# Optimization experiments

Hardware: AMD Instinct MI355X
Metric: run time of the kernel (lower is better)

The kernel has to match this reference:

```python
import jax, jax.numpy as jnp
import numpy as np
from jax import lax

BN_EPS = 1e-3  # keras BatchNormalization default

def _conv(x, w):
    # x: (N,H,W,Cin), w: (kh,kw,Cin,Cout), 'same' padding, stride 1
    return lax.conv_general_dilated(x, w, (1, 1), 'SAME',
                                    dimension_numbers=('NHWC', 'HWIO', 'NHWC'))

def _hard_sigmoid(x):  # keras ConvLSTM2D default recurrent_activation
    return jnp.clip(0.2 * x + 0.5, 0.0, 1.0)

def _convlstm(x, Wx, Wh, b, return_sequences):
    # x: (B,T,H,W,Cin); Wx: (3,3,Cin,4F); Wh: (3,3,F,4F); gates order i,f,c,o
    B, T, H, W, Cin = x.shape
    F = Wh.shape[2]
    # precompute input-to-gate convs for all timesteps at once (one big conv)
    gx = _conv(x.reshape(B * T, H, W, Cin), Wx) + b
    gx = gx.reshape(B, T, H, W, 4 * F).transpose(1, 0, 2, 3, 4)  # (T,B,H,W,4F)
    h0 = jnp.zeros((B, H, W, F), x.dtype)
    c0 = jnp.zeros((B, H, W, F), x.dtype)

    def step(carry, gxt):
        h, c = carry
        z = gxt + _conv(h, Wh)
        zi, zf, zc, zo = jnp.split(z, 4, axis=-1)
        c = _hard_sigmoid(zf) * c + _hard_sigmoid(zi) * jnp.tanh(zc)
        h = _hard_sigmoid(zo) * jnp.tanh(c)
        return (h, c), h

    (hT, _), hs = lax.scan(step, (h0, c0), gx)
    if return_sequences:
        return hs.transpose(1, 0, 2, 3, 4)  # (B,T,H,W,F)
    return hT  # (B,H,W,F)

def _bn(x, gamma, beta, mean, var):
    return (x - mean) * (gamma * lax.rsqrt(var + BN_EPS)) + beta

def _pool_thw(x):  # MaxPool3D(pool_size=(1,2,2))
    B, T, H, W, C = x.shape
    return x.reshape(B, T, H // 2, 2, W // 2, 2, C).max(axis=(3, 5))

def _pool_hw(x):  # MaxPool2D()
    B, H, W, C = x.shape
    return x.reshape(B, H // 2, 2, W // 2, 2, C).max(axis=(2, 4))

def setup_inputs() -> dict:
    key = jax.random.key(0)
    ks = jax.random.split(key, 16)
    s = 0.05  # weight scale
    d = {
        'x':   jax.random.normal(ks[0], (8, 12, 64, 64, 3), jnp.float32),
        'W1x': jax.random.normal(ks[1], (3, 3, 3, 64), jnp.float32) * s,
        'W1h': jax.random.normal(ks[2], (3, 3, 16, 64), jnp.float32) * s,
        'b1':  jnp.zeros((64,), jnp.float32),
        'g1':  jnp.ones((16,), jnp.float32),
        'be1': jnp.zeros((16,), jnp.float32),
        'm1':  jax.random.normal(ks[3], (16,), jnp.float32) * 0.1,
        'v1':  jax.random.uniform(ks[4], (16,), jnp.float32) + 0.5,
        'W2x': jax.random.normal(ks[5], (3, 3, 16, 128), jnp.float32) * s,
        'W2h': jax.random.normal(ks[6], (3, 3, 32, 128), jnp.float32) * s,
        'b2':  jnp.zeros((128,), jnp.float32),
        'g2':  jnp.ones((32,), jnp.float32),
        'be2': jnp.zeros((32,), jnp.float32),
        'm2':  jax.random.normal(ks[7], (32,), jnp.float32) * 0.1,
        'v2':  jax.random.uniform(ks[8], (32,), jnp.float32) + 0.5,
        'W3x': jax.random.normal(ks[9], (3, 3, 32, 256), jnp.float32) * s,
        'W3h': jax.random.normal(ks[10], (3, 3, 64, 256), jnp.float32) * s,
        'b3':  jnp.zeros((256,), jnp.float32),
        'Wd1': jax.random.normal(ks[11], (4096, 10000), jnp.float32) * 0.01,
        'bd1': jnp.zeros((10000,), jnp.float32),
        'Wd2': jax.random.normal(ks[12], (10000, 1000), jnp.float32) * 0.01,
        'bd2': jnp.zeros((1000,), jnp.float32),
        'Wd3': jax.random.normal(ks[13], (1000, 100), jnp.float32) * 0.03,
        'bd3': jnp.zeros((100,), jnp.float32),
        'Wd4': jax.random.normal(ks[14], (100, 10), jnp.float32) * 0.1,
        'bd4': jnp.zeros((10,), jnp.float32),
        'Wc':  jax.random.normal(ks[15], (10, 1), jnp.float32) * 0.3,
        'bc':  jnp.zeros((1,), jnp.float32),
    }
    return d

def reference(x, W1x, W1h, b1, g1, be1, m1, v1,
              W2x, W2h, b2, g2, be2, m2, v2,
              W3x, W3h, b3,
              Wd1, bd1, Wd2, bd2, Wd3, bd3, Wd4, bd4, Wc, bc):
    h = _convlstm(x, W1x, W1h, b1, True)          # (B,12,64,64,16)
    h = _bn(h, g1, be1, m1, v1)
    h = _pool_thw(h)                              # (B,12,32,32,16)
    h = _convlstm(h, W2x, W2h, b2, True)          # (B,12,32,32,32)
    h = _bn(h, g2, be2, m2, v2)
    h = _pool_thw(h)                              # (B,12,16,16,32)
    h = _convlstm(h, W3x, W3h, b3, False)         # (B,16,16,64)
    h = _pool_hw(h)                               # (B,8,8,64)
    h = h.reshape(h.shape[0], -1)                 # (B,4096)
    h = h @ Wd1 + bd1
    h = h @ Wd2 + bd2
    h = h @ Wd3 + bd3
    h = h @ Wd4 + bd4
    return h @ Wc + bc                            # (B,1)
```

## Files before the change

### kernel.cpp

```cpp
#include <hip/hip_runtime.h>
#include <hip/hip_bf16.h>
#include <math.h>

__global__ void transpose_wx(const float* __restrict__ src, float* __restrict__ dst,
                             int Cin, int CinP, int Cout)
{
  int i = blockIdx.x * 256 + threadIdx.x;
  int total = 9 * Cout * CinP;
  if (i >= total) return;
  int j = i & 3; int rem = i >> 2;
  int co = rem % Cout; rem /= Cout;
  int c4c = rem % (CinP / 4); int tap = rem / (CinP / 4);
  int c = c4c * 4 + j;
  dst[i] = (c < Cin) ? src[((size_t)tap * Cin + c) * Cout + co] : 0.f;
}

__global__ void transpose_wh(const float* __restrict__ src, float* __restrict__ dst, int F)
{
  int i = blockIdx.x * 256 + threadIdx.x;
  int total = 9 * 4 * F * F;
  if (i >= total) return;
  int j = i & 3; int rem = i >> 2;
  int f = rem % F; rem /= F;
  int c4c = rem % (F / 4); rem /= (F / 4);
  int g = rem & 3; int tap = rem >> 2;
  int c = c4c * 4 + j;
  dst[i] = src[((size_t)tap * F + c) * 4 * F + g * F + f];
}

template<int H, int W, int Cin, int Cout, int TH, int TW, int COL, int NG>
__global__ __launch_bounds__(256) void conv3x3_bias(
    const float* __restrict__ in, const float* __restrict__ wtT,
    const float* __restrict__ bias, float* __restrict__ out)
{
  static_assert(COL * NG == Cout, "cout coverage");
  constexpr int CIN_P = (Cin % 4 == 0) ? Cin : ((Cin + 3) / 4) * 4;
  constexpr int TILES_X = W / TW, TILES_Y = H / TH;
  constexpr int PAD_W = TW + 2, PAD_H = TH + 2;
  constexpr int LDS_N = PAD_H * PAD_W * CIN_P;
  constexpr int NPG = 256 / COL;
  constexpr int PPT = TH * TW / NPG;
  __shared__ __align__(16) float tile[LDS_N];

  int blk = blockIdx.x;
  int n = blk / (TILES_X * TILES_Y);
  int trem = blk % (TILES_X * TILES_Y);
  int ty = trem / TILES_X, tx = trem % TILES_X;
  int y0 = ty * TH, x0 = tx * TW;
  const float* inN = in + (size_t)n * H * W * Cin;

  for (int i = threadIdx.x; i < LDS_N; i += 256) {
    int ci = i % CIN_P; int rem = i / CIN_P;
    int xx = rem % PAD_W; int yy = rem / PAD_W;
    int gy = y0 + yy - 1, gx = x0 + xx - 1;
    float v = 0.f;
    if (ci < Cin && gy >= 0 && gy < H && gx >= 0 && gx < W)
      v = inN[((size_t)gy * W + gx) * Cin + ci];
    tile[i] = v;
  }
  __syncthreads();

  int cobase = threadIdx.x % COL;
  int pg = threadIdx.x / COL;
  float* outN = out + (size_t)n * H * W * Cout;

  float acc[NG][PPT];
#pragma unroll
  for (int g = 0; g < NG; ++g) {
    float bco = bias[g * COL + cobase];
#pragma unroll
    for (int j = 0; j < PPT; ++j) acc[g][j] = bco;
  }

  const float4* wt4 = (const float4*)wtT;
#pragma unroll
  for (int kh = 0; kh < 3; ++kh)
#pragma unroll
  for (int kw = 0; kw < 3; ++kw) {
    const float4* wtap = wt4 + (size_t)(kh * 3 + kw) * (CIN_P / 4) * Cout;
#pragma unroll 1
    for (int c4 = 0; c4 < CIN_P; c4 += 4) {
      const float4* wrow = wtap + (size_t)(c4 / 4) * Cout + cobase;
      float4 w[NG];
#pragma unroll
      for (int g = 0; g < NG; ++g) w[g] = wrow[g * COL];
#pragma unroll
      for (int j = 0; j < PPT; ++j) {
        int p = pg * PPT + j;
        int ly = p / TW, lx = p % TW;
        const float4 h4 = *(const float4*)&tile[((ly + kh) * PAD_W + (lx + kw)) * CIN_P + c4];
#pragma unroll
        for (int g = 0; g < NG; ++g)
          acc[g][j] += h4.x * w[g].x + h4.y * w[g].y + h4.z * w[g].z + h4.w * w[g].w;
      }
    }
  }

#pragma unroll
  for (int j = 0; j < PPT; ++j) {
    int p = pg * PPT + j;
    int ly = p / TW, lx = p % TW;
    float* op = &outN[((size_t)(y0 + ly) * W + (x0 + lx)) * Cout + cobase];
#pragma unroll
    for (int g = 0; g < NG; ++g) op[g * COL] = acc[g][j];
  }
}

__device__ __forceinline__ float hsig(float x) {
  return fminf(fmaxf(0.2f * x + 0.5f, 0.f), 1.f);
}

template<int H, int W, int F, int TH, int TW>
__global__ __launch_bounds__(256) void lstm_step(
    const float* __restrict__ gx, long gx_bstride,
    const float* __restrict__ hprev, long hp_bstride,
    const float* __restrict__ whT,
    float* __restrict__ c,
    float* __restrict__ hout, long ho_bstride,
    int first)
{
  constexpr int TILES_X = W / TW, TILES_Y = H / TH;
  constexpr int PAD_W = TW + 2, PAD_H = TH + 2;
  constexpr int LDS_N = PAD_H * PAD_W * F;
  __shared__ __align__(16) float tile[LDS_N];

  int blk = blockIdx.x;
  int b = blk / (TILES_X * TILES_Y);
  int trem = blk % (TILES_X * TILES_Y);
  int ty = trem / TILES_X, tx = trem % TILES_X;
  int y0 = ty * TH, x0 = tx * TW;

  if (first) {
    for (int i = threadIdx.x; i < LDS_N; i += 256) tile[i] = 0.f;
  } else {
    const float* hb = hprev + (size_t)b * hp_bstride;
    for (int i = threadIdx.x; i < LDS_N; i += 256) {
      int ci = i % F; int rem = i / F;
      int xx = rem % PAD_W, yy = rem / PAD_W;
      int gy = y0 + yy - 1, gxp = x0 + xx - 1;
      float v = 0.f;
      if (gy >= 0 && gy < H && gxp >= 0 && gxp < W)
        v = hb[((size_t)gy * W + gxp) * F + ci];
      tile[i] = v;
    }
  }
  __syncthreads();

  constexpr int G = 256 / F;
  constexpr int P = TH * TW;
  constexpr int NP = P / G;
  int f = threadIdx.x % F;
  int pg = threadIdx.x / F;

  float acc[4][NP];
  const float* gxb = gx + (size_t)b * gx_bstride;
#pragma unroll
  for (int j = 0; j < NP; ++j) {
    int p = pg * NP + j;
    int gy = y0 + p / TW, gxp = x0 + p % TW;
    size_t base = ((size_t)gy * W + gxp) * 4 * F;
#pragma unroll
    for (int g = 0; g < 4; ++g) acc[g][j] = gxb[base + g * F + f];
  }

  const float4* wh4 = (const float4*)whT;
#pragma unroll
  for (int kh = 0; kh < 3; ++kh)
#pragma unroll
  for (int kw = 0; kw < 3; ++kw) {
    int tap = kh * 3 + kw;
#pragma unroll 1
    for (int c4 = 0; c4 < F; c4 += 4) {
      float4 h4[NP];
#pragma unroll
      for (int j = 0; j < NP; ++j) {
        int p = pg * NP + j;
        int ly = p / TW, lx = p % TW;
        h4[j] = *(const float4*)&tile[((ly + kh) * PAD_W + (lx + kw)) * F + c4];
      }
      float4 w0 = wh4[((size_t)(tap * 4 + 0) * (F / 4) + c4 / 4) * F + f];
      float4 w1 = wh4[((size_t)(tap * 4 + 1) * (F / 4) + c4 / 4) * F + f];
      float4 w2 = wh4[((size_t)(tap * 4 + 2) * (F / 4) + c4 / 4) * F + f];
      float4 w3 = wh4[((size_t)(tap * 4 + 3) * (F / 4) + c4 / 4) * F + f];
#pragma unroll
      for (int j = 0; j < NP; ++j) {
        acc[0][j] += h4[j].x * w0.x + h4[j].y * w0.y + h4[j].z * w0.z + h4[j].w * w0.w;
        acc[1][j] += h4[j].x * w1.x + h4[j].y * w1.y + h4[j].z * w1.z + h4[j].w * w1.w;
        acc[2][j] += h4[j].x * w2.x + h4[j].y * w2.y + h4[j].z * w2.z + h4[j].w * w2.w;
        acc[3][j] += h4[j].x * w3.x + h4[j].y * w3.y + h4[j].z * w3.z + h4[j].w * w3.w;
      }
    }
  }

  float* cb = c + (size_t)b * H * W * F;
  float* hb2 = hout + (size_t)b * ho_bstride;
#pragma unroll
  for (int j = 0; j < NP; ++j) {
    int p = pg * NP + j;
    int gy = y0 + p / TW, gxp = x0 + p % TW;
    size_t idx = ((size_t)gy * W + gxp) * F + f;
    float zi = acc[0][j], zf = acc[1][j], zc = acc[2][j], zo = acc[3][j];
    float cold = first ? 0.f : cb[idx];
    float cn = hsig(zf) * cold + hsig(zi) * tanhf(zc);
    cb[idx] = cn;
    hb2[idx] = hsig(zo) * tanhf(cn);
  }
}

__global__ void bnpool_kernel(const float* __restrict__ in,
                              const float* __restrict__ g, const float* __restrict__ be,
                              const float* __restrict__ m, const float* __restrict__ v,
                              float* __restrict__ out, int total, int H, int W, int F)
{
  int i = blockIdx.x * 256 + threadIdx.x;
  if (i >= total) return;
  int f = i % F; int rem = i / F;
  int x = rem % (W / 2); rem /= (W / 2);
  int y = rem % (H / 2); int nt = rem / (H / 2);
  float scale = g[f] * rsqrtf(v[f] + 1e-3f);
  float shift = be[f] - m[f] * scale;
  const float* base = in + (((size_t)nt * H + 2 * y) * W + 2 * x) * F + f;
  float a0 = base[0] * scale + shift;
  float a1 = base[F] * scale + shift;
  float a2 = base[(size_t)W * F] * scale + shift;
  float a3 = base[(size_t)W * F + F] * scale + shift;
  out[i] = fmaxf(fmaxf(a0, a1), fmaxf(a2, a3));
}

__global__ void poolhw_kernel(const float* __restrict__ in, float* __restrict__ out, int total)
{
  int i = blockIdx.x * 256 + threadIdx.x;
  if (i >= total) return;
  int f = i % 64; int rem = i / 64;
  int x = rem % 8; rem /= 8;
  int y = rem % 8; int b = rem / 8;
  const float* base = in + (((size_t)b * 16 + 2 * y) * 16 + 2 * x) * 64 + f;
  float a0 = base[0], a1 = base[64], a2 = base[16 * 64], a3 = base[16 * 64 + 64];
  out[i] = fmaxf(fmaxf(a0, a1), fmaxf(a2, a3));
}

__global__ __launch_bounds__(256) void dense_partial(
    const float* __restrict__ x, const float* __restrict__ w,
    float* __restrict__ part, int K, int N, int kchunk)
{
  extern __shared__ __align__(16) float xs[];
  int kb = blockIdx.y;
  int k0 = kb * kchunk;
  int klen = min(kchunk, K - k0);
  for (int i = threadIdx.x; i < klen * 8; i += 256) {
    int kk = i >> 3, b = i & 7;
    xs[i] = x[(size_t)b * K + k0 + kk];
  }
  __syncthreads();
  int co = blockIdx.x * 256 + threadIdx.x;
  if (co >= N) return;
  float acc[8];
#pragma unroll
  for (int b = 0; b < 8; ++b) acc[b] = 0.f;
  const float4* xs4 = (const float4*)xs;
  const float* wp = w + (size_t)k0 * N + co;
#pragma unroll 4
  for (int kk = 0; kk < klen; ++kk) {
    float wv = wp[(size_t)kk * N];
    float4 lo = xs4[kk * 2], hi = xs4[kk * 2 + 1];
    acc[0] += lo.x * wv; acc[1] += lo.y * wv;
    acc[2] += lo.z * wv; acc[3] += lo.w * wv;
    acc[4] += hi.x * wv; acc[5] += hi.y * wv;
    acc[6] += hi.z * wv; acc[7] += hi.w * wv;
  }
#pragma unroll
  for (int b = 0; b < 8; ++b)
    part[((size_t)kb * 8 + b) * N + co] = acc[b];
}

__global__ __launch_bounds__(256) void dense_reduce(
    const float* __restrict__ part, const float* __restrict__ bias,
    float* __restrict__ out, int N, int S)
{
  int co = blockIdx.x * 256 + threadIdx.x;
  int b = blockIdx.y;
  if (co >= N) return;
  float acc = bias[co];
#pragma unroll 4
  for (int kb = 0; kb < S; ++kb)
    acc += part[((size_t)kb * 8 + b) * N + co];
  out[(size_t)b * N + co] = acc;
}

__global__ void dense_small(const float* __restrict__ x, const float* __restrict__ w,
                            const float* __restrict__ bias, float* __restrict__ out,
                            int K, int N, int total)
{
  int idx = blockIdx.x * 256 + threadIdx.x;
  if (idx >= total) return;
  int b = idx / N, co = idx % N;
  float acc = bias[co];
  const float* xb = x + (size_t)b * K;
#pragma unroll 4
  for (int k = 0; k < K; ++k) acc += xb[k] * w[(size_t)k * N + co];
  out[idx] = acc;
}

__global__ void dense_tail(const float* __restrict__ d3,
                           const float* __restrict__ w4, const float* __restrict__ b4,
                           const float* __restrict__ wc, const float* __restrict__ bc,
                           float* __restrict__ out)
{
  __shared__ float d4[8][10];
  int t = threadIdx.x;
  if (t < 80) {
    int b = t / 10, co = t % 10;
    float acc = b4[co];
    for (int k = 0; k < 100; ++k) acc += d3[b * 100 + k] * w4[k * 10 + co];
    d4[b][co] = acc;
  }
  __syncthreads();
  if (t < 8) {
    float acc = bc[0];
    for (int j = 0; j < 10; ++j) acc += d4[t][j] * wc[j];
    out[t] = acc;
  }
}

extern "C" void kernel_launch(void* const* d_in, const int* in_sizes, int n_in,
                              void* d_out, int out_size, void* d_ws, size_t ws_size,
                              hipStream_t stream)
{
  const float* x   = (const float*)d_in[0];
  const float* W1x = (const float*)d_in[1];
  const float* W1h = (const float*)d_in[2];
  const float* b1  = (const float*)d_in[3];
  const float* g1  = (const float*)d_in[4];
  const float* be1 = (const float*)d_in[5];
  const float* m1  = (const float*)d_in[6];
  const float* v1  = (const float*)d_in[7];
  const float* W2x = (const float*)d_in[8];
  const float* W2h = (const float*)d_in[9];
  const float* b2  = (const float*)d_in[10];
  const float* g2  = (const float*)d_in[11];
  const float* be2 = (const float*)d_in[12];
  const float* m2  = (const float*)d_in[13];
  const float* v2  = (const float*)d_in[14];
  const float* W3x = (const float*)d_in[15];
  const float* W3h = (const float*)d_in[16];
  const float* b3  = (const float*)d_in[17];
  const float* Wd1 = (const float*)d_in[18];
  const float* bd1 = (const float*)d_in[19];
  const float* Wd2 = (const float*)d_in[20];
  const float* bd2 = (const float*)d_in[21];
  const float* Wd3 = (const float*)d_in[22];
  const float* bd3 = (const float*)d_in[23];
  const float* Wd4 = (const float*)d_in[24];
  const float* bd4 = (const float*)d_in[25];
  const float* Wc  = (const float*)d_in[26];
  const float* bc  = (const float*)d_in[27];

  char* ws = (char*)d_ws;
  size_t off = 0;
  auto alloc = [&](size_t bytes) { size_t r = off; off = (off + bytes + 255) & ~(size_t)255; return r; };
  size_t oR0    = alloc(100663296);
  size_t oR1    = alloc(25165824);
  size_t oR2    = alloc(6291456);
  size_t oR3    = alloc(2097152);
  size_t oh3a   = alloc(524288);
  size_t oh3b   = alloc(524288);
  size_t oflat  = alloc(131072);
  size_t od1    = alloc(320000);
  size_t od2    = alloc(32000);
  size_t od3    = alloc(3200);
  size_t oWx1T  = alloc(9216);
  size_t oWx2T  = alloc(73728);
  size_t oWx3T  = alloc(294912);
  size_t oWh1T  = alloc(36864);
  size_t oWh2T  = alloc(147456);
  size_t oWh3T  = alloc(589824);
  (void)ws_size; (void)in_sizes; (void)n_in; (void)out_size;

  float* gx1   = (float*)(ws + oR0);
  float* gx2   = (float*)(ws + oR0);
  float* gx3   = (float*)(ws + oR0);
  float* part1 = (float*)(ws + oR0);
  float* part2 = (float*)(ws + oR0 + 33554432);
  float* hseq1 = (float*)(ws + oR1);
  float* hseq2 = (float*)(ws + oR1);
  float* pool1 = (float*)(ws + oR2);
  float* pool2 = (float*)(ws + oR2);
  float* cbuf  = (float*)(ws + oR3);
  float* h3a   = (float*)(ws + oh3a);
  float* h3b   = (float*)(ws + oh3b);
  float* flat  = (float*)(ws + oflat);
  float* d1    = (float*)(ws + od1);
  float* d2    = (float*)(ws + od2);
  float* d3b   = (float*)(ws + od3);
  float* Wx1T  = (float*)(ws + oWx1T);
  float* Wx2T  = (float*)(ws + oWx2T);
  float* Wx3T  = (float*)(ws + oWx3T);
  float* Wh1T  = (float*)(ws + oWh1T);
  float* Wh2T  = (float*)(ws + oWh2T);
  float* Wh3T  = (float*)(ws + oWh3T);

  const int B = 8, T = 12;

  transpose_wx<<<(9 * 64 * 4 + 255) / 256, 256, 0, stream>>>(W1x, Wx1T, 3, 4, 64);
  transpose_wx<<<(9 * 128 * 16 + 255) / 256, 256, 0, stream>>>(W2x, Wx2T, 16, 16, 128);
  transpose_wx<<<(9 * 256 * 32 + 255) / 256, 256, 0, stream>>>(W3x, Wx3T, 32, 32, 256);
  transpose_wh<<<(9 * 4 * 16 * 16 + 255) / 256, 256, 0, stream>>>(W1h, Wh1T, 16);
  transpose_wh<<<(9 * 4 * 32 * 32 + 255) / 256, 256, 0, stream>>>(W2h, Wh2T, 32);
  transpose_wh<<<(9 * 4 * 64 * 64 + 255) / 256, 256, 0, stream>>>(W3h, Wh3T, 64);

  conv3x3_bias<64, 64, 3, 64, 4, 8, 32, 2><<<96 * 128, 256, 0, stream>>>(x, Wx1T, b1, gx1);
  {
    const long gxs = (long)T * 64 * 64 * 64;
    const long hs  = (long)T * 64 * 64 * 16;
    for (int t = 0; t < T; ++t) {
      lstm_step<64, 64, 16, 8, 8><<<B * 64, 256, 0, stream>>>(
          gx1 + (size_t)t * 64 * 64 * 64, gxs,
          t ? hseq1 + (size_t)(t - 1) * 64 * 64 * 16 : nullptr, hs,
          Wh1T, cbuf, hseq1 + (size_t)t * 64 * 64 * 16, hs, t == 0);
    }
  }
  {
    int total = B * T * 32 * 32 * 16;
    bnpool_kernel<<<(total + 255) / 256, 256, 0, stream>>>(hseq1, g1, be1, m1, v1, pool1, total, 64, 64, 16);
  }

  conv3x3_bias<32, 32, 16, 128, 4, 8, 32, 4><<<96 * 32, 256, 0, stream>>>(pool1, Wx2T, b2, gx2);
  {
    const long gxs = (long)T * 32 * 32 * 128;
    const long hs  = (long)T * 32 * 32 * 32;
    for (int t = 0; t < T; ++t) {
      lstm_step<32, 32, 32, 4, 4><<<B * 64, 256, 0, stream>>>(
          gx2 + (size_t)t * 32 * 32 * 128, gxs,
          t ? hseq2 + (size_t)(t - 1) * 32 * 32 * 32 : nullptr, hs,
          Wh2T, cbuf, hseq2 + (size_t)t * 32 * 32 * 32, hs, t == 0);
    }
  }
  {
    int total = B * T * 16 * 16 * 32;
    bnpool_kernel<<<(total + 255) / 256, 256, 0, stream>>>(hseq2, g2, be2, m2, v2, pool2, total, 32, 32, 32);
  }

  conv3x3_bias<16, 16, 32, 256, 4, 8, 64, 4><<<96 * 8, 256, 0, stream>>>(pool2, Wx3T, b3, gx3);
  {
    const long gxs = (long)T * 16 * 16 * 256;
    const long hs  = (long)16 * 16 * 64;
    for (int t = 0; t < T; ++t) {
      float* hout = (t % 2 == 0) ? h3a : h3b;
      const float* hp = (t % 2 == 0) ? h3b : h3a;
      lstm_step<16, 16, 64, 2, 4><<<B * 32, 256, 0, stream>>>(
          gx3 + (size_t)t * 16 * 16 * 256, gxs,
          t ? hp : nullptr, hs,
          Wh3T, cbuf, hout, hs, t == 0);
    }
  }
  poolhw_kernel<<<(32768 + 255) / 256, 256, 0, stream>>>(h3b, flat, 32768);

  dense_partial<<<dim3(40, 64), 256, 64 * 8 * 4, stream>>>(flat, Wd1, part1, 4096, 10000, 64);
  dense_reduce<<<dim3(40, 8), 256, 0, stream>>>(part1, bd1, d1, 10000, 64);
  dense_partial<<<dim3(4, 125), 256, 80 * 8 * 4, stream>>>(d1, Wd2, part2, 10000, 1000, 80);
  dense_reduce<<<dim3(4, 8), 256, 0, stream>>>(part2, bd2, d2, 1000, 125);
  dense_small<<<(800 + 255) / 256, 256, 0, stream>>>(d2, Wd3, bd3, d3b, 1000, 100, 800);
  dense_tail<<<1, 128, 0, stream>>>(d3b, Wd4, bd4, Wc, bc, (float*)d_out);
}
```

Before: 1.518 ms.

## Fuse ConvLSTM timesteps into persistent kernels with grid-wide atomic barriers

Replaces the per-timestep lstm_step launches with one persistent lstm_layer kernel per layer that loops over all 12 timesteps and synchronises blocks through an atomic counter barrier in global memory. The goal is to remove 36 kernel launches and their launch gaps. The six weight-transpose kernels become a single launch, and the third dense layer becomes a split-K partial/reduce pair. The grid barrier only works if every block is resident at once; the grids are 512 and 256 blocks with launch_bounds(256,2), so a co-residency failure would deadlock.

```diff
diff --git a/kernel.cpp b/kernel.cpp
--- a/kernel.cpp
+++ b/kernel.cpp
@@ -2,12 +2,10 @@
 #include <hip/hip_bf16.h>
 #include <math.h>
 
-__global__ void transpose_wx(const float* __restrict__ src, float* __restrict__ dst,
-                             int Cin, int CinP, int Cout)
-{
-  int i = blockIdx.x * 256 + threadIdx.x;
-  int total = 9 * Cout * CinP;
-  if (i >= total) return;
+__device__ __forceinline__ void wx_elem(const float* __restrict__ src,
+                                        float* __restrict__ dst, int i,
+                                        int Cin, int CinP, int Cout)
+{
   int j = i & 3; int rem = i >> 2;
   int co = rem % Cout; rem /= Cout;
   int c4c = rem % (CinP / 4); int tap = rem / (CinP / 4);
@@ -15,17 +13,31 @@
   dst[i] = (c < Cin) ? src[((size_t)tap * Cin + c) * Cout + co] : 0.f;
 }
 
-__global__ void transpose_wh(const float* __restrict__ src, float* __restrict__ dst, int F)
-{
-  int i = blockIdx.x * 256 + threadIdx.x;
-  int total = 9 * 4 * F * F;
-  if (i >= total) return;
+__device__ __forceinline__ void wh_elem(const float* __restrict__ src,
+                                        float* __restrict__ dst, int i, int F)
+{
   int j = i & 3; int rem = i >> 2;
   int f = rem % F; rem /= F;
   int c4c = rem % (F / 4); rem /= (F / 4);
   int g = rem & 3; int tap = rem >> 2;
   int c = c4c * 4 + j;
   dst[i] = src[((size_t)tap * F + c) * 4 * F + g * F + f];
+}
+
+__global__ void transpose_all(
+    const float* __restrict__ W1x, const float* __restrict__ W2x,
+    const float* __restrict__ W3x, const float* __restrict__ W1h,
+    const float* __restrict__ W2h, const float* __restrict__ W3h,
+    float* __restrict__ Wx1T, float* __restrict__ Wx2T, float* __restrict__ Wx3T,
+    float* __restrict__ Wh1T, float* __restrict__ Wh2T, float* __restrict__ Wh3T)
+{
+  int i = blockIdx.x * 256 + threadIdx.x;
+  if (i < 2304)        wx_elem(W1x, Wx1T, i,          3,  4,  64);
+  else if (i < 20736)  wx_elem(W2x, Wx2T, i - 2304,   16, 16, 128);
+  else if (i < 94464)  wx_elem(W3x, Wx3T, i - 20736,  32, 32, 256);
+  else if (i < 103680) wh_elem(W1h, Wh1T, i - 94464,  16);
+  else if (i < 140544) wh_elem(W2h, Wh2T, i - 103680, 32);
+  else if (i < 288000) wh_elem(W3h, Wh3T, i - 140544, 64);
 }
 
 template<int H, int W, int Cin, int Cout, int TH, int TW, int COL, int NG>
@@ -110,14 +122,13 @@
   return fminf(fmaxf(0.2f * x + 0.5f, 0.f), 1.f);
 }
 
-template<int H, int W, int F, int TH, int TW>
-__global__ __launch_bounds__(256) void lstm_step(
+template<int H, int W, int F, int TH, int TW, int TSEQ>
+__global__ __launch_bounds__(256, 2) void lstm_layer(
     const float* __restrict__ gx, long gx_bstride,
-    const float* __restrict__ hprev, long hp_bstride,
     const float* __restrict__ whT,
     float* __restrict__ c,
-    float* __restrict__ hout, long ho_bstride,
-    int first)
+    float* __restrict__ hseq, long h_bstride,
+    unsigned int* __restrict__ bar)
 {
   constexpr int TILES_X = W / TW, TILES_Y = H / TH;
   constexpr int PAD_W = TW + 2, PAD_H = TH + 2;
@@ -130,80 +141,97 @@
   int ty = trem / TILES_X, tx = trem % TILES_X;
   int y0 = ty * TH, x0 = tx * TW;
 
-  if (first) {
-    for (int i = threadIdx.x; i < LDS_N; i += 256) tile[i] = 0.f;
-  } else {
-    const float* hb = hprev + (size_t)b * hp_bstride;
-    for (int i = threadIdx.x; i < LDS_N; i += 256) {
-      int ci = i % F; int rem = i / F;
-      int xx = rem % PAD_W, yy = rem / PAD_W;
-      int gy = y0 + yy - 1, gxp = x0 + xx - 1;
-      float v = 0.f;
-      if (gy >= 0 && gy < H && gxp >= 0 && gxp < W)
-        v = hb[((size_t)gy * W + gxp) * F + ci];
-      tile[i] = v;
-    }
-  }
-  __syncthreads();
-
   constexpr int G = 256 / F;
   constexpr int P = TH * TW;
   constexpr int NP = P / G;
   int f = threadIdx.x % F;
   int pg = threadIdx.x / F;
 
-  float acc[4][NP];
-  const float* gxb = gx + (size_t)b * gx_bstride;
-#pragma unroll
-  for (int j = 0; j < NP; ++j) {
-    int p = pg * NP + j;
-    int gy = y0 + p / TW, gxp = x0 + p % TW;
-    size_t base = ((size_t)gy * W + gxp) * 4 * F;
-#pragma unroll
-    for (int g = 0; g < 4; ++g) acc[g][j] = gxb[base + g * F + f];
-  }
-
   const float4* wh4 = (const float4*)whT;
-#pragma unroll
-  for (int kh = 0; kh < 3; ++kh)
-#pragma unroll
-  for (int kw = 0; kw < 3; ++kw) {
-    int tap = kh * 3 + kw;
+  float* cb = c + (size_t)b * H * W * F;
+
 #pragma unroll 1
-    for (int c4 = 0; c4 < F; c4 += 4) {
-      float4 h4[NP];
-#pragma unroll
-      for (int j = 0; j < NP; ++j) {
-        int p = pg * NP + j;
-        int ly = p / TW, lx = p % TW;
-        h4[j] = *(const float4*)&tile[((ly + kh) * PAD_W + (lx + kw)) * F + c4];
+  for (int t = 0; t < TSEQ; ++t) {
+    if (t == 0) {
+      for (int i = threadIdx.x; i < LDS_N; i += 256) tile[i] = 0.f;
+    } else {
+      const float* hb = hseq + (size_t)b * h_bstride + (size_t)(t - 1) * H * W * F;
+      for (int i = threadIdx.x; i < LDS_N; i += 256) {
+        int ci = i % F; int rem = i / F;
+        int xx = rem % PAD_W, yy = rem / PAD_W;
+        int gy = y0 + yy - 1, gxp = x0 + xx - 1;
+        float v = 0.f;
+        if (gy >= 0 && gy < H && gxp >= 0 && gxp < W)
+          v = hb[((size_t)gy * W + gxp) * F + ci];
+        tile[i] = v;
       }
-      float4 w0 = wh4[((size_t)(tap * 4 + 0) * (F / 4) + c4 / 4) * F + f];
-      float4 w1 = wh4[((size_t)(tap * 4 + 1) * (F / 4) + c4 / 4) * F + f];
-      float4 w2 = wh4[((size_t)(tap * 4 + 2) * (F / 4) + c4 / 4) * F + f];
-      float4 w3 = wh4[((size_t)(tap * 4 + 3) * (F / 4) + c4 / 4) * F + f];
-#pragma unroll
-      for (int j = 0; j < NP; ++j) {
-        acc[0][j] += h4[j].x * w0.x + h4[j].y * w0.y + h4[j].z * w0.z + h4[j].w * w0.w;
-        acc[1][j] += h4[j].x * w1.x + h4[j].y * w1.y + h4[j].z * w1.z + h4[j].w * w1.w;
-        acc[2][j] += h4[j].x * w2.x + h4[j].y * w2.y + h4[j].z * w2.z + h4[j].w * w2.w;
-        acc[3][j] += h4[j].x * w3.x + h4[j].y * w3.y + h4[j].z * w3.z + h4[j].w * w3.w;
+    }
+    __syncthreads();
+
+    float acc[4][NP];
+    const float* gxb = gx + (size_t)b * gx_bstride + (size_t)t * H * W * 4 * F;
+#pragma unroll
+    for (int j = 0; j < NP; ++j) {
+      int p = pg * NP + j;
+      int gy = y0 + p / TW, gxp = x0 + p % TW;
+      size_t base = ((size_t)gy * W + gxp) * 4 * F;
+#pragma unroll
+      for (int g = 0; g < 4; ++g) acc[g][j] = gxb[base + g * F + f];
+    }
+
+#pragma unroll
+    for (int kh = 0; kh < 3; ++kh)
+#pragma unroll
+    for (int kw = 0; kw < 3; ++kw) {
+      int tap = kh * 3 + kw;
+#pragma unroll 1
+      for (int c4 = 0; c4 < F; c4 += 4) {
+        float4 h4[NP];
+#pragma unroll
+        for (int j = 0; j < NP; ++j) {
+          int p = pg * NP + j;
+          int ly = p / TW, lx = p % TW;
+          h4[j] = *(const float4*)&tile[((ly + kh) * PAD_W + (lx + kw)) * F + c4];
+        }
+        float4 w0 = wh4[((size_t)(tap * 4 + 0) * (F / 4) + c4 / 4) * F + f];
+        float4 w1 = wh4[((size_t)(tap * 4 + 1) * (F / 4) + c4 / 4) * F + f];
+        float4 w2 = wh4[((size_t)(tap * 4 + 2) * (F / 4) + c4 / 4) * F + f];
+        float4 w3 = wh4[((size_t)(tap * 4 + 3) * (F / 4) + c4 / 4) * F + f];
+#pragma unroll
+        for (int j = 0; j < NP; ++j) {
+          acc[0][j] += h4[j].x * w0.x + h4[j].y * w0.y + h4[j].z * w0.z + h4[j].w * w0.w;
+          acc[1][j] += h4[j].x * w1.x + h4[j].y * w1.y + h4[j].z * w1.z + h4[j].w * w1.w;
+          acc[2][j] += h4[j].x * w2.x + h4[j].y * w2.y + h4[j].z * w2.z + h4[j].w * w2.w;
+          acc[3][j] += h4[j].x * w3.x + h4[j].y * w3.y + h4[j].z * w3.z + h4[j].w * w3.w;
+        }
       }
     }
-  }
-
-  float* cb = c + (size_t)b * H * W * F;
-  float* hb2 = hout + (size_t)b * ho_bstride;
-#pragma unroll
-  for (int j = 0; j < NP; ++j) {
-    int p = pg * NP + j;
-    int gy = y0 + p / TW, gxp = x0 + p % TW;
-    size_t idx = ((size_t)gy * W + gxp) * F + f;
-    float zi = acc[0][j], zf = acc[1][j], zc = acc[2][j], zo = acc[3][j];
-    float cold = first ? 0.f : cb[idx];
-    float cn = hsig(zf) * cold + hsig(zi) * tanhf(zc);
-    cb[idx] = cn;
-    hb2[idx] = hsig(zo) * tanhf(cn);
+
+    float* hb2 = hseq + (size_t)b * h_bstride + (size_t)t * H * W * F;
+#pragma unroll
+    for (int j = 0; j < NP; ++j) {
+      int p = pg * NP + j;
+      int gy = y0 + p / TW, gxp = x0 + p % TW;
+      size_t idx = ((size_t)gy * W + gxp) * F + f;
+      float zi = acc[0][j], zf = acc[1][j], zc = acc[2][j], zo = acc[3][j];
+      float cold = (t == 0) ? 0.f : cb[idx];
+      float cn = hsig(zf) * cold + hsig(zi) * tanhf(zc);
+      cb[idx] = cn;
+      hb2[idx] = hsig(zo) * tanhf(cn);
+    }
+
+    if (t < TSEQ - 1) {
+      __syncthreads();
+      if (threadIdx.x == 0) {
+        __threadfence();
+        __hip_atomic_fetch_add(&bar[t], 1u, __ATOMIC_RELEASE, __HIP_MEMORY_SCOPE_AGENT);
+        while (__hip_atomic_load(&bar[t], __ATOMIC_ACQUIRE, __HIP_MEMORY_SCOPE_AGENT)
+               < (unsigned)gridDim.x)
+          __builtin_amdgcn_s_sleep(8);
+        __threadfence();
+      }
+      __syncthreads();
+    }
   }
 }
 
@@ -227,14 +255,15 @@
   out[i] = fmaxf(fmaxf(a0, a1), fmaxf(a2, a3));
 }
 
-__global__ void poolhw_kernel(const float* __restrict__ in, float* __restrict__ out, int total)
+__global__ void poolhw_kernel(const float* __restrict__ in, float* __restrict__ out,
+                              int total, long bstride)
 {
   int i = blockIdx.x * 256 + threadIdx.x;
   if (i >= total) return;
   int f = i % 64; int rem = i / 64;
   int x = rem % 8; rem /= 8;
   int y = rem % 8; int b = rem / 8;
-  const float* base = in + (((size_t)b * 16 + 2 * y) * 16 + 2 * x) * 64 + f;
+  const float* base = in + (size_t)b * bstride + (((size_t)2 * y) * 16 + 2 * x) * 64 + f;
   float a0 = base[0], a1 = base[64], a2 = base[16 * 64], a3 = base[16 * 64 + 64];
   out[i] = fmaxf(fmaxf(a0, a1), fmaxf(a2, a3));
 }
@@ -287,37 +316,32 @@
   out[(size_t)b * N + co] = acc;
 }
 
-__global__ void dense_small(const float* __restrict__ x, const float* __restrict__ w,
-                            const float* __restrict__ bias, float* __restrict__ out,
-                            int K, int N, int total)
-{
-  int idx = blockIdx.x * 256 + threadIdx.x;
-  if (idx >= total) return;
-  int b = idx / N, co = idx % N;
-  float acc = bias[co];
-  const float* xb = x + (size_t)b * K;
-#pragma unroll 4
-  for (int k = 0; k < K; ++k) acc += xb[k] * w[(size_t)k * N + co];
-  out[idx] = acc;
-}
-
 __global__ void dense_tail(const float* __restrict__ d3,
                            const float* __restrict__ w4, const float* __restrict__ b4,
                            const float* __restrict__ wc, const float* __restrict__ bc,
                            float* __restrict__ out)
 {
+  __shared__ float sd3[800];
+  __shared__ float sw4[1000];
+  __shared__ float swc[10];
   __shared__ float d4[8][10];
   int t = threadIdx.x;
+  for (int i = t; i < 800; i += 256) sd3[i] = d3[i];
+  for (int i = t; i < 1000; i += 256) sw4[i] = w4[i];
+  if (t < 10) swc[t] = wc[t];
+  __syncthreads();
   if (t < 80) {
     int b = t / 10, co = t % 10;
     float acc = b4[co];
-    for (int k = 0; k < 100; ++k) acc += d3[b * 100 + k] * w4[k * 10 + co];
+#pragma unroll 4
+    for (int k = 0; k < 100; ++k) acc += sd3[b * 100 + k] * sw4[k * 10 + co];
     d4[b][co] = acc;
   }
   __syncthreads();
   if (t < 8) {
     float acc = bc[0];
-    for (int j = 0; j < 10; ++j) acc += d4[t][j] * wc[j];
+#pragma unroll
+    for (int j = 0; j < 10; ++j) acc += d4[t][j] * swc[j];
     out[t] = acc;
   }
 }
@@ -362,18 +386,18 @@
   size_t oR1    = alloc(25165824);
   size_t oR2    = alloc(6291456);
   size_t oR3    = alloc(2097152);
-  size_t oh3a   = alloc(524288);
-  size_t oh3b   = alloc(524288);
   size_t oflat  = alloc(131072);
   size_t od1    = alloc(320000);
   size_t od2    = alloc(32000);
   size_t od3    = alloc(3200);
+  size_t opart3 = alloc(64000);
   size_t oWx1T  = alloc(9216);
   size_t oWx2T  = alloc(73728);
   size_t oWx3T  = alloc(294912);
   size_t oWh1T  = alloc(36864);
   size_t oWh2T  = alloc(147456);
   size_t oWh3T  = alloc(589824);
+  size_t ocnt   = alloc(144);
   (void)ws_size; (void)in_sizes; (void)n_in; (void)out_size;
 
   float* gx1   = (float*)(ws + oR0);
@@ -383,82 +407,56 @@
   float* part2 = (float*)(ws + oR0 + 33554432);
   float* hseq1 = (float*)(ws + oR1);
   float* hseq2 = (float*)(ws + oR1);
+  float* hseq3 = (float*)(ws + oR1);
   float* pool1 = (float*)(ws + oR2);
   float* pool2 = (float*)(ws + oR2);
   float* cbuf  = (float*)(ws + oR3);
-  float* h3a   = (float*)(ws + oh3a);
-  float* h3b   = (float*)(ws + oh3b);
   float* flat  = (float*)(ws + oflat);
   float* d1    = (float*)(ws + od1);
   float* d2    = (float*)(ws + od2);
   float* d3b   = (float*)(ws + od3);
+  float* part3 = (float*)(ws + opart3);
   float* Wx1T  = (float*)(ws + oWx1T);
   float* Wx2T  = (float*)(ws + oWx2T);
   float* Wx3T  = (float*)(ws + oWx3T);
   float* Wh1T  = (float*)(ws + oWh1T);
   float* Wh2T  = (float*)(ws + oWh2T);
   float* Wh3T  = (float*)(ws + oWh3T);
+  unsigned int* cnt = (unsigned int*)(ws + ocnt);
 
   const int B = 8, T = 12;
 
-  transpose_wx<<<(9 * 64 * 4 + 255) / 256, 256, 0, stream>>>(W1x, Wx1T, 3, 4, 64);
-  transpose_wx<<<(9 * 128 * 16 + 255) / 256, 256, 0, stream>>>(W2x, Wx2T, 16, 16, 128);
-  transpose_wx<<<(9 * 256 * 32 + 255) / 256, 256, 0, stream>>>(W3x, Wx3T, 32, 32, 256);
-  transpose_wh<<<(9 * 4 * 16 * 16 + 255) / 256, 256, 0, stream>>>(W1h, Wh1T, 16);
-  transpose_wh<<<(9 * 4 * 32 * 32 + 255) / 256, 256, 0, stream>>>(W2h, Wh2T, 32);
-  transpose_wh<<<(9 * 4 * 64 * 64 + 255) / 256, 256, 0, stream>>>(W3h, Wh3T, 64);
+  hipMemsetAsync(cnt, 0, 144, stream);
+  transpose_all<<<1125, 256, 0, stream>>>(W1x, W2x, W3x, W1h, W2h, W3h,
+                                          Wx1T, Wx2T, Wx3T, Wh1T, Wh2T, Wh3T);
 
   conv3x3_bias<64, 64, 3, 64, 4, 8, 32, 2><<<96 * 128, 256, 0, stream>>>(x, Wx1T, b1, gx1);
-  {
-    const long gxs = (long)T * 64 * 64 * 64;
-    const long hs  = (long)T * 64 * 64 * 16;
-    for (int t = 0; t < T; ++t) {
-      lstm_step<64, 64, 16, 8, 8><<<B * 64, 256, 0, stream>>>(
-          gx1 + (size_t)t * 64 * 64 * 64, gxs,
-          t ? hseq1 + (size_t)(t - 1) * 64 * 64 * 16 : nullptr, hs,
-          Wh1T, cbuf, hseq1 + (size_t)t * 64 * 64 * 16, hs, t == 0);
-    }
-  }
+  lstm_layer<64, 64, 16, 8, 8, 12><<<B * 64, 256, 0, stream>>>(
+      gx1, (long)T * 64 * 64 * 64, Wh1T, cbuf, hseq1, (long)T * 64 * 64 * 16, cnt + 0);
   {
     int total = B * T * 32 * 32 * 16;
     bnpool_kernel<<<(total + 255) / 256, 256, 0, stream>>>(hseq1, g1, be1, m1, v1, pool1, total, 64, 64, 16);
   }
 
   conv3x3_bias<32, 32, 16, 128, 4, 8, 32, 4><<<96 * 32, 256, 0, stream>>>(pool1, Wx2T, b2, gx2);
-  {
-    const long gxs = (long)T * 32 * 32 * 128;
-    const long hs  = (long)T * 32 * 32 * 32;
-    for (int t = 0; t < T; ++t) {
-      lstm_step<32, 32, 32, 4, 4><<<B * 64, 256, 0, stream>>>(
-          gx2 + (size_t)t * 32 * 32 * 128, gxs,
-          t ? hseq2 + (size_t)(t - 1) * 32 * 32 * 32 : nullptr, hs,
-          Wh2T, cbuf, hseq2 + (size_t)t * 32 * 32 * 32, hs, t == 0);
-    }
-  }
+  lstm_layer<32, 32, 32, 4, 4, 12><<<B * 64, 256, 0, stream>>>(
+      gx2, (long)T * 32 * 32 * 128, Wh2T, cbuf, hseq2, (long)T * 32 * 32 * 32, cnt + 12);
   {
     int total = B * T * 16 * 16 * 32;
     bnpool_kernel<<<(total + 255) / 256, 256, 0, stream>>>(hseq2, g2, be2, m2, v2, pool2, total, 32, 32, 32);
   }
 
   conv3x3_bias<16, 16, 32, 256, 4, 8, 64, 4><<<96 * 8, 256, 0, stream>>>(pool2, Wx3T, b3, gx3);
-  {
-    const long gxs = (long)T * 16 * 16 * 256;
-    const long hs  = (long)16 * 16 * 64;
-    for (int t = 0; t < T; ++t) {
-      float* hout = (t % 2 == 0) ? h3a : h3b;
-      const float* hp = (t % 2 == 0) ? h3b : h3a;
-      lstm_step<16, 16, 64, 2, 4><<<B * 32, 256, 0, stream>>>(
-          gx3 + (size_t)t * 16 * 16 * 256, gxs,
-          t ? hp : nullptr, hs,
-          Wh3T, cbuf, hout, hs, t == 0);
-    }
-  }
-  poolhw_kernel<<<(32768 + 255) / 256, 256, 0, stream>>>(h3b, flat, 32768);
+  lstm_layer<16, 16, 64, 2, 4, 12><<<B * 32, 256, 0, stream>>>(
+      gx3, (long)T * 16 * 16 * 256, Wh3T, cbuf, hseq3, (long)T * 16 * 16 * 64, cnt + 24);
+  poolhw_kernel<<<(32768 + 255) / 256, 256, 0, stream>>>(
+      hseq3 + (size_t)11 * 16 * 16 * 64, flat, 32768, (long)T * 16 * 16 * 64);
 
   dense_partial<<<dim3(40, 64), 256, 64 * 8 * 4, stream>>>(flat, Wd1, part1, 4096, 10000, 64);
   dense_reduce<<<dim3(40, 8), 256, 0, stream>>>(part1, bd1, d1, 10000, 64);
   dense_partial<<<dim3(4, 125), 256, 80 * 8 * 4, stream>>>(d1, Wd2, part2, 10000, 1000, 80);
   dense_reduce<<<dim3(4, 8), 256, 0, stream>>>(part2, bd2, d2, 1000, 125);
-  dense_small<<<(800 + 255) / 256, 256, 0, stream>>>(d2, Wd3, bd3, d3b, 1000, 100, 800);
-  dense_tail<<<1, 128, 0, stream>>>(d3b, Wd4, bd4, Wc, bc, (float*)d_out);
-}
+  dense_partial<<<dim3(1, 20), 256, 50 * 8 * 4, stream>>>(d2, Wd3, part3, 1000, 100, 50);
+  dense_reduce<<<dim3(1, 8), 256, 0, stream>>>(part3, bd3, d3b, 100, 20);
+  dense_tail<<<1, 256, 0, stream>>>(d3b, Wd4, bd4, Wc, bc, (float*)d_out);
+}
```

Result: slower. 3.309 ms (+118.0%).
